# Kernel tuning notes

Hardware: AMD Instinct MI355X
Metric: run time of the kernel (lower is better)

The kernel has to match this reference:

```python
import jax, jax.numpy as jnp
import numpy as np


def _layernorm(x, g, b, eps=1e-5):
    m = jnp.mean(x, axis=-1, keepdims=True)
    v = jnp.var(x, axis=-1, keepdims=True)
    return (x - m) / jnp.sqrt(v + eps) * g + b


def _gat_layer(x, W, a1, a2, Wo, bo, diag_mask):
    # x: [B,N,D]; W: [H,D,D]; a1,a2: [H,D]; Wo: [H*D,D]; bo: [D]
    # Additive-attention split: a.[h_i;h_j] = a1.h_i + a2.h_j (same math as
    # the torch concat+linear, since the score layer is linear and bias-free).
    h = jnp.einsum('bni,hio->bhno', x, W)                       # [B,H,N,D]
    s1 = jnp.einsum('bhnd,hd->bhn', h, a1)                      # [B,H,N]
    s2 = jnp.einsum('bhnd,hd->bhn', h, a2)                      # [B,H,N]
    e = jax.nn.leaky_relu(s1[..., :, None] + s2[..., None, :], 0.2)  # [B,H,N,N]
    # fully-connected adjacency = ones - eye -> mask only the diagonal
    e = jnp.where(diag_mask, -jnp.inf, e)
    alpha = jax.nn.softmax(e, axis=-1)                          # [B,H,N,N]
    out = jnp.einsum('bhij,bhjd->bhid', alpha, h)               # [B,H,N,D]
    B, H, N, D = out.shape
    out = out.transpose(0, 2, 1, 3).reshape(B, N, H * D)        # concat heads
    return out @ Wo + bo                                        # [B,N,D]


def setup_inputs() -> dict:
    key = jax.random.key(0)
    ks = jax.random.split(key, 9)
    B, N, IN, D, H, L = 16, 1024, 7, 128, 4, 3
    s = 0.1
    return {
        'node_features': jax.random.normal(ks[0], (B, N, IN), jnp.float32),
        'Wp': jax.random.normal(ks[1], (IN, D), jnp.float32) * s,
        'bp': jax.random.normal(ks[2], (D,), jnp.float32) * s,
        'W':  jax.random.normal(ks[3], (L, H, D, D), jnp.float32) * s,
        'a1': jax.random.normal(ks[4], (L, H, D), jnp.float32) * s,
        'a2': jax.random.normal(ks[5], (L, H, D), jnp.float32) * s,
        'Wo': jax.random.normal(ks[6], (L, H * D, D), jnp.float32) * s,
        'bo': jax.random.normal(ks[7], (L, D), jnp.float32) * s,
        'gamma': jnp.ones((L, D), jnp.float32),
        'beta': jnp.zeros((L, D), jnp.float32),
    }


def reference(node_features, Wp, bp, W, a1, a2, Wo, bo, gamma, beta):
    B, N, _ = node_features.shape
    L = W.shape[0]
    diag_mask = jnp.eye(N, dtype=bool)  # adjacency==0 positions of (ones-eye)
    x = node_features @ Wp + bp         # input_proj
    for i in range(L):
        x_new = _gat_layer(x, W[i], a1[i], a2[i], Wo[i], bo[i], diag_mask)
        if i > 0:
            x = _layernorm(x + x_new, gamma[i], beta[i])  # residual + LN
        else:
            x = _layernorm(x_new, gamma[i], beta[i])
        if i < L - 1:
            x = jax.nn.relu(x)
    return x
```

## Files before the change

### kernel.cpp

```cpp
#include <hip/hip_runtime.h>
#include <hip/hip_bf16.h>

typedef __attribute__((ext_vector_type(8))) _Float16 f16x8;
typedef __attribute__((ext_vector_type(2))) _Float16 f16x2;
typedef __attribute__((ext_vector_type(8))) short short8;
typedef __attribute__((ext_vector_type(4))) short short4v;
typedef __attribute__((ext_vector_type(4))) float f32x4;

#define LDP 72
#define LDH 64

typedef const __attribute__((address_space(1))) unsigned int* gas_ptr;
typedef __attribute__((address_space(3))) unsigned int* las_ptr;
#define GLDS16(gp, lp) \
  __builtin_amdgcn_global_load_lds((gas_ptr)(gp), (las_ptr)(lp), 16, 0, 0)

#if __has_builtin(__builtin_amdgcn_fdot2)
#define FDOT2(a, b, c) __builtin_amdgcn_fdot2((a), (b), (c), false)
#else
__device__ __forceinline__ float FDOT2(f16x2 a, f16x2 b, float c) {
  return c + (float)a[0] * (float)b[0] + (float)a[1] * (float)b[1];
}
#endif

union h8u {
  f16x8 v;
  f16x2 h[4];
};

__device__ __forceinline__ short f2h(float f) {
  union { _Float16 h; short s; } u; u.h = (_Float16)f; return u.s;
}
__device__ __forceinline__ float h2f(short s) {
  union { short s; _Float16 h; } u; u.s = s; return (float)u.h;
}

__global__ __launch_bounds__(256) void k_tw(const float* __restrict__ W,
                                            const float* __restrict__ Wo,
                                            short* __restrict__ WT,
                                            short* __restrict__ WoT) {
  int idx = blockIdx.x * 256 + threadIdx.x;
  if (idx < 3 * 512 * 128) {
    int l = idx >> 16, rem = idx & 65535;
    int c = rem >> 7, k = rem & 127;
    int h = c >> 7, o = c & 127;
    WT[idx] = f2h(W[(((l * 4 + h) * 128 + k) << 7) + o]);
  } else {
    int j = idx - 3 * 512 * 128;
    int l = j >> 16, rem = j & 65535;
    int d = rem >> 9, c = rem & 511;
    WoT[j] = f2h(Wo[((l * 512 + c) << 7) + d]);
  }
}

__global__ __launch_bounds__(256) void k_inproj(const float* __restrict__ nf,
                                                const float* __restrict__ Wp,
                                                const float* __restrict__ bp,
                                                short* __restrict__ xh) {
  int idx = blockIdx.x * 256 + threadIdx.x;
  int bn = idx >> 7, d = idx & 127;
  float acc = bp[d];
  const float* nr = nf + bn * 7;
#pragma unroll
  for (int i = 0; i < 7; ++i) acc += nr[i] * Wp[(i << 7) + d];
  xh[idx] = f2h(acc);
}

__global__ __launch_bounds__(256) void k_gemm_h(const short* __restrict__ xh,
                                                const short* __restrict__ WT,
                                                short* __restrict__ hT,
                                                const float* __restrict__ a1,
                                                const float* __restrict__ a2,
                                                float* __restrict__ s1g,
                                                float* __restrict__ s2g) {
  __shared__ __align__(16) short As[128 * LDP];
  __shared__ __align__(16) short Bs[128 * LDP];
  __shared__ float sred[2][2][128];
  const int t = threadIdx.x;
  const int bn0 = blockIdx.x << 7;
  const int head = blockIdx.y;
  const int c0 = head << 7;
  const int w = t >> 6, lane = t & 63, lr = lane & 15, lq = lane >> 4;
  const int wr = w >> 1, wc = w & 1;
  f32x4 acc[4][4] = {};
  for (int k0 = 0; k0 < 128; k0 += 64) {
    const int row = t >> 1, half = (t & 1) << 5;
    {
      const short* sa = xh + ((bn0 + row) << 7) + k0 + half;
      short* da = As + row * LDP + half;
      *(short8*)(da) = *(const short8*)(sa);
      *(short8*)(da + 8) = *(const short8*)(sa + 8);
      *(short8*)(da + 16) = *(const short8*)(sa + 16);
      *(short8*)(da + 24) = *(const short8*)(sa + 24);
      const short* sb = WT + ((c0 + row) << 7) + k0 + half;
      short* db = Bs + row * LDP + half;
      *(short8*)(db) = *(const short8*)(sb);
      *(short8*)(db + 8) = *(const short8*)(sb + 8);
      *(short8*)(db + 16) = *(const short8*)(sb + 16);
      *(short8*)(db + 24) = *(const short8*)(sb + 24);
    }
    __syncthreads();
#pragma unroll
    for (int kk = 0; kk < 2; ++kk) {
      f16x8 a[4], b[4];
#pragma unroll
      for (int m = 0; m < 4; ++m)
        a[m] = *(const f16x8*)(As + (wr * 64 + m * 16 + lr) * LDP + (kk << 5) + (lq << 3));
#pragma unroll
      for (int n = 0; n < 4; ++n)
        b[n] = *(const f16x8*)(Bs + (wc * 64 + n * 16 + lr) * LDP + (kk << 5) + (lq << 3));
#pragma unroll
      for (int m = 0; m < 4; ++m)
#pragma unroll
        for (int n = 0; n < 4; ++n)
          acc[m][n] = __builtin_amdgcn_mfma_f32_16x16x32_f16(a[m], b[n], acc[m][n], 0, 0, 0);
    }
    __syncthreads();
  }
  const int b = bn0 >> 10;
  const int nb = bn0 & 1023;
  float a1v[4], a2v[4];
#pragma unroll
  for (int n = 0; n < 4; ++n) {
    int d = wc * 64 + n * 16 + lr;
    a1v[n] = a1[(head << 7) + d];
    a2v[n] = a2[(head << 7) + d];
  }
#pragma unroll
  for (int m = 0; m < 4; ++m)
#pragma unroll
    for (int r = 0; r < 4; ++r) {
      float v1 = 0.f, v2 = 0.f;
#pragma unroll
      for (int n = 0; n < 4; ++n) {
        v1 += acc[m][n][r] * a1v[n];
        v2 += acc[m][n][r] * a2v[n];
      }
#pragma unroll
      for (int off = 1; off < 16; off <<= 1) {
        v1 += __shfl_xor(v1, off);
        v2 += __shfl_xor(v2, off);
      }
      if (lr == 0) {
        int row = wr * 64 + m * 16 + (lq << 2) + r;
        sred[wc][0][row] = v1;
        sred[wc][1][row] = v2;
      }
    }
#pragma unroll
  for (int m = 0; m < 4; ++m) {
    int nrow = nb + wr * 64 + m * 16 + (lq << 2);
#pragma unroll
    for (int n = 0; n < 4; ++n) {
      int d = wc * 64 + n * 16 + lr;
      long base = ((long)((((b << 2) + head) << 7) + d) << 10) + nrow;
      short4v v;
      v[0] = f2h(acc[m][n][0]); v[1] = f2h(acc[m][n][1]);
      v[2] = f2h(acc[m][n][2]); v[3] = f2h(acc[m][n][3]);
      *(short4v*)(hT + base) = v;
    }
  }
  __syncthreads();
  {
    const int bh_ = (b << 2) + head;
    if (t < 128)
      s1g[(bh_ << 10) + nb + t] = sred[0][0][t] + sred[1][0][t];
    else
      s2g[(bh_ << 10) + nb + (t - 128)] = sred[0][1][t - 128] + sred[1][1][t - 128];
  }
}

__global__ __launch_bounds__(256) void k_ef(const float* __restrict__ s2g,
                                            float* __restrict__ s2m,
                                            short* __restrict__ Eh,
                                            short* __restrict__ Fh) {
  const int bh = blockIdx.x, t = threadIdx.x;
  __shared__ float red[4];
  f32x4 v = *(const f32x4*)&s2g[(bh << 10) + (t << 2)];
  float mx = fmaxf(fmaxf(v[0], v[1]), fmaxf(v[2], v[3]));
#pragma unroll
  for (int off = 1; off < 64; off <<= 1) mx = fmaxf(mx, __shfl_xor(mx, off));
  if ((t & 63) == 0) red[t >> 6] = mx;
  __syncthreads();
  const float smax = fmaxf(fmaxf(red[0], red[1]), fmaxf(red[2], red[3]));
  if (t == 0) s2m[bh] = smax;
  short4v e, f;
#pragma unroll
  for (int q = 0; q < 4; ++q) {
    e[q] = f2h(__expf(v[q] - smax));
    f[q] = f2h(__expf(0.2f * (v[q] - smax)));
  }
  *(short4v*)&Eh[(bh << 10) + (t << 2)] = e;
  *(short4v*)&Fh[(bh << 10) + (t << 2)] = f;
}

__global__ __launch_bounds__(256) void k_attn(const short* __restrict__ hT,
                                              const float* __restrict__ s1,
                                              const short* __restrict__ Eh,
                                              const short* __restrict__ Fh,
                                              const float* __restrict__ s2max,
                                              short* __restrict__ attn) {
  __shared__ __align__(16) short Hs[2][128 * LDH];
  __shared__ __align__(16) _Float16 Esh[1024];
  __shared__ __align__(16) _Float16 Fsh[1024];
  const int bh = blockIdx.x, it = blockIdx.y;
  const int i0 = it << 7;
  const int t = threadIdx.x;
  const int w = t >> 6, lane = t & 63, lr = lane & 15, lq = lane >> 4;

  const short* hTb = hT + ((long)bh << 17);
  const int grow = (w << 5) + (lane >> 3);
  const int gcol = ((lane & 7) ^ (lane >> 3)) << 3;
  const short* gsrc = hTb + ((long)grow << 10) + gcol;

#define STAGE(buf, J0)                                             \
  do {                                                             \
    short* ldsb = &Hs[buf][(w << 5) << 6];                         \
    _Pragma("unroll") for (int i_ = 0; i_ < 4; ++i_)               \
        GLDS16(gsrc + ((long)(i_ << 3) << 10) + (J0),              \
               ldsb + ((i_ << 3) << 6));                           \
  } while (0)

  STAGE(0, 0);
  *(short4v*)&Esh[t << 2] = *(const short4v*)&Eh[(bh << 10) + (t << 2)];
  *(short4v*)&Fsh[t << 2] = *(const short4v*)&Fh[(bh << 10) + (t << 2)];

  const float smax = s2max[bh];
  f16x8 Ai8[2], Bi8[2];
  const f16x2 one2 = {(_Float16)1.f, (_Float16)1.f};
  f16x8 dmask[2];
  float dsum[2] = {0.f, 0.f};
#pragma unroll
  for (int m = 0; m < 2; ++m) {
    const int rblk = (w << 5) + (m << 4) + lr;
    float s1v = s1[(bh << 10) + i0 + rblk];
    float x = s1v + smax;
    float mi = fmaxf(x, 0.2f * x);
    _Float16 A_ = (_Float16)__expf(x - mi);
    _Float16 B_ = (_Float16)__expf(0.2f * x - mi);
#pragma unroll
    for (int e = 0; e < 8; ++e) { Ai8[m][e] = A_; Bi8[m][e] = B_; }
    const int lqz = ((m << 1) + (lr >> 3)) & 3, ez = lr & 7;
#pragma unroll
    for (int e = 0; e < 8; ++e)
      dmask[m][e] = (lq == lqz && e == ez) ? (_Float16)0.f : (_Float16)1.f;
  }
  const int jtd = (it << 1) + (w >> 1);
  const int kkd = w & 1;
  f32x4 acc[2][8] = {};
  __syncthreads();

#define TILE(buf, jt, DIAG)                                                    \
  do {                                                                         \
    _Pragma("unroll") for (int kk = 0; kk < 2; ++kk) {                         \
      const int ebase = ((jt) << 6) + (kk << 5) + (lq << 3);                   \
      f16x8 ev8 = *(const f16x8*)&Esh[ebase];                                  \
      f16x8 fv8 = *(const f16x8*)&Fsh[ebase];                                  \
      f16x8 bf[8];                                                             \
      _Pragma("unroll") for (int n = 0; n < 8; ++n) {                          \
        const int r_ = (n << 4) + lr;                                          \
        const int slot_ = ((kk << 2) + lq) ^ (r_ & 7);                         \
        bf[n] = *(const f16x8*)(&Hs[buf][(r_ << 6) + (slot_ << 3)]);           \
      }                                                                        \
      f16x8 af[2];                                                             \
      _Pragma("unroll") for (int m = 0; m < 2; ++m) {                          \
        f16x8 pm = __builtin_elementwise_max(Ai8[m] * ev8, Bi8[m] * fv8);      \
        if ((DIAG) && kk == kkd) pm = pm * dmask[m];                           \
        af[m] = pm;                                                            \
        h8u u_; u_.v = pm;                                                     \
        _Pragma("unroll") for (int p = 0; p < 4; ++p)                          \
            dsum[m] = FDOT2(u_.h[p], one2, dsum[m]);                           \
      }                                                                        \
      _Pragma("unroll") for (int m = 0; m < 2; ++m)                            \
        _Pragma("unroll") for (int n = 0; n < 8; ++n)                          \
            acc[m][n] = __builtin_amdgcn_mfma_f32_16x16x32_f16(                \
                af[m], bf[n], acc[m][n], 0, 0, 0);                             \
    }                                                                          \
  } while (0)

#pragma unroll 1
  for (int jt2 = 0; jt2 < 8; ++jt2) {
    const int jA = jt2 << 1, jB = jA | 1;
    STAGE(1, jB << 6);
    __builtin_amdgcn_s_setprio(1);
    TILE(0, jA, jA == jtd);
    __builtin_amdgcn_s_setprio(0);
    __syncthreads();
    if (jt2 < 7) STAGE(0, (jA + 2) << 6);
    __builtin_amdgcn_s_setprio(1);
    TILE(1, jB, jB == jtd);
    __builtin_amdgcn_s_setprio(0);
    __syncthreads();
  }

  const int b = bh >> 2, head = bh & 3;
#pragma unroll
  for (int m = 0; m < 2; ++m) {
    float s = dsum[m];
    s += __shfl_xor(s, 16);
    s += __shfl_xor(s, 32);
    float rs = 1.f / s;
    f32x4 d4;
#pragma unroll
    for (int q = 0; q < 4; ++q)
      d4[q] = __shfl(rs, (lane & 48) | ((lq << 2) + q));
    int irow = i0 + (w << 5) + (m << 4) + (lq << 2);
#pragma unroll
    for (int n = 0; n < 8; ++n) {
      int d = (n << 4) + lr;
      long base = ((long)((b << 10) + irow) << 9) + (head << 7) + d;
      attn[base] = f2h(acc[m][n][0] * d4[0]);
      attn[base + 512] = f2h(acc[m][n][1] * d4[1]);
      attn[base + 1024] = f2h(acc[m][n][2] * d4[2]);
      attn[base + 1536] = f2h(acc[m][n][3] * d4[3]);
    }
  }
#undef STAGE
#undef TILE
}

template <int HAS_RES, int DO_RELU, int WRITE_OUT>
__global__ __launch_bounds__(256) void k_outproj(const short* __restrict__ attn,
                                                 const short* __restrict__ WoT,
                                                 const float* __restrict__ bo,
                                                 const float* __restrict__ gamma,
                                                 const float* __restrict__ beta,
                                                 float* __restrict__ xf,
                                                 short* __restrict__ xh,
                                                 float* __restrict__ outp) {
  __shared__ __align__(16) short As[64 * LDP];
  __shared__ __align__(16) short Bs[128 * LDP];
  const int t = threadIdx.x;
  const int bn0 = blockIdx.x << 6;
  const int w = t >> 6, lane = t & 63, lr = lane & 15, lq = lane >> 4;
  f32x4 acc[8] = {};
  const int rowA = t >> 2, chA = (t & 3) << 4;
  const int rowB = t >> 1, chB = (t & 1) << 5;
  for (int k0 = 0; k0 < 512; k0 += 64) {
    {
      const short* sa = attn + ((long)(bn0 + rowA) << 9) + k0 + chA;
      short* da = As + rowA * LDP + chA;
      *(short8*)(da) = *(const short8*)(sa);
      *(short8*)(da + 8) = *(const short8*)(sa + 8);
      const short* sb = WoT + (rowB << 9) + k0 + chB;
      short* db = Bs + rowB * LDP + chB;
      *(short8*)(db) = *(const short8*)(sb);
      *(short8*)(db + 8) = *(const short8*)(sb + 8);
      *(short8*)(db + 16) = *(const short8*)(sb + 16);
      *(short8*)(db + 24) = *(const short8*)(sb + 24);
    }
    __syncthreads();
#pragma unroll
    for (int kk = 0; kk < 2; ++kk) {
      f16x8 a = *(const f16x8*)(As + ((w << 4) + lr) * LDP + (kk << 5) + (lq << 3));
#pragma unroll
      for (int n = 0; n < 8; ++n) {
        f16x8 b = *(const f16x8*)(Bs + ((n << 4) + lr) * LDP + (kk << 5) + (lq << 3));
        acc[n] = __builtin_amdgcn_mfma_f32_16x16x32_f16(a, b, acc[n], 0, 0, 0);
      }
    }
    __syncthreads();
  }
  float v[8][4], gam[8], bet[8];
#pragma unroll
  for (int n = 0; n < 8; ++n) {
    int d = (n << 4) + lr;
    float bv = bo[d];
    gam[n] = gamma[d];
    bet[n] = beta[d];
#pragma unroll
    for (int r = 0; r < 4; ++r) {
      float x = acc[n][r] + bv;
      if (HAS_RES) x += xf[((bn0 + (w << 4) + (lq << 2) + r) << 7) + d];
      v[n][r] = x;
    }
  }
#pragma unroll
  for (int r = 0; r < 4; ++r) {
    float s = 0.f, q = 0.f;
#pragma unroll
    for (int n = 0; n < 8; ++n) { s += v[n][r]; q += v[n][r] * v[n][r]; }
#pragma unroll
    for (int mk = 1; mk < 16; mk <<= 1) { s += __shfl_xor(s, mk); q += __shfl_xor(q, mk); }
    float mean = s * 0.0078125f;
    float var = q * 0.0078125f - mean * mean;
    float rstd = rsqrtf(var + 1e-5f);
    int row = bn0 + (w << 4) + (lq << 2) + r;
#pragma unroll
    for (int n = 0; n < 8; ++n) {
      int d = (n << 4) + lr;
      float o = (v[n][r] - mean) * rstd * gam[n] + bet[n];
      if (DO_RELU) o = fmaxf(o, 0.f);
      if (WRITE_OUT) {
        outp[(row << 7) + d] = o;
      } else {
        xh[(row << 7) + d] = f2h(o);
        xf[(row << 7) + d] = o;
      }
    }
  }
}

extern "C" void kernel_launch(void* const* d_in, const int* in_sizes, int n_in,
                              void* d_out, int out_size, void* d_ws, size_t ws_size,
                              hipStream_t stream) {
  const float* nf = (const float*)d_in[0];
  const float* Wp = (const float*)d_in[1];
  const float* bp = (const float*)d_in[2];
  const float* W = (const float*)d_in[3];
  const float* a1 = (const float*)d_in[4];
  const float* a2 = (const float*)d_in[5];
  const float* Wo = (const float*)d_in[6];
  const float* bo = (const float*)d_in[7];
  const float* gamma = (const float*)d_in[8];
  const float* beta = (const float*)d_in[9];
  float* outp = (float*)d_out;

  char* ws = (char*)d_ws;
  short* xh = (short*)(ws);
  float* xf = (float*)(ws + (4ll << 20));
  short* hT = (short*)(ws + (12ll << 20));
  short* attn = (short*)(ws + (28ll << 20));
  float* s1 = (float*)(ws + (44ll << 20));
  float* s2g = (float*)(ws + (44ll << 20) + (256ll << 10));
  short* Eh = (short*)(ws + (44ll << 20) + (512ll << 10));
  short* Fh = (short*)(ws + (44ll << 20) + (640ll << 10));
  float* s2m = (float*)(ws + (44ll << 20) + (768ll << 10));
  short* WT = (short*)(ws + (45ll << 20));
  short* WoT = (short*)(ws + (45ll << 20) + 393216);

  k_tw<<<1536, 256, 0, stream>>>(W, Wo, WT, WoT);
  k_inproj<<<8192, 256, 0, stream>>>(nf, Wp, bp, xh);
  for (int l = 0; l < 3; ++l) {
    k_gemm_h<<<dim3(128, 4), 256, 0, stream>>>(xh, WT + l * 65536, hT,
                                               a1 + l * 512, a2 + l * 512, s1, s2g);
    k_ef<<<64, 256, 0, stream>>>(s2g, s2m, Eh, Fh);
    k_attn<<<dim3(64, 8), 256, 0, stream>>>(hT, s1, Eh, Fh, s2m, attn);
    if (l == 0)
      k_outproj<0, 1, 0><<<256, 256, 0, stream>>>(attn, WoT + l * 65536, bo + l * 128,
                                                  gamma + l * 128, beta + l * 128, xf, xh, outp);
    else if (l == 1)
      k_outproj<1, 1, 0><<<256, 256, 0, stream>>>(attn, WoT + l * 65536, bo + l * 128,
                                                  gamma + l * 128, beta + l * 128, xf, xh, outp);
    else
      k_outproj<1, 0, 1><<<256, 256, 0, stream>>>(attn, WoT + l * 65536, bo + l * 128,
                                                  gamma + l * 128, beta + l * 128, xf, xh, outp);
  }
}
```

Baseline: 170.8 us.

## Triple-buffer attention H tiles and split outproj rows across more blocks

The attention kernel moves from double to triple buffering of the H tiles in LDS. It prefetches two tiles ahead and replaces __syncthreads with explicit vmcnt waits and raw barriers, so global-to-LDS loads overlap more MFMA work. The output projection kernel halves the rows per block, from 64 to 32, and splits the 128 output columns across wave pairs. The LayerNorm statistics are then combined through shared memory, and twice as many blocks are launched. The changes trade extra LDS use and an added cross-wave reduction barrier for deeper latency hiding and better occupancy across CUs.

```diff
diff --git a/kernel.cpp b/kernel.cpp
--- a/kernel.cpp
+++ b/kernel.cpp
@@ -200,7 +200,7 @@
                                               const short* __restrict__ Fh,
                                               const float* __restrict__ s2max,
                                               short* __restrict__ attn) {
-  __shared__ __align__(16) short Hs[2][128 * LDH];
+  __shared__ __align__(16) short Hs[3][128 * LDH];
   __shared__ __align__(16) _Float16 Esh[1024];
   __shared__ __align__(16) _Float16 Fsh[1024];
   const int bh = blockIdx.x, it = blockIdx.y;
@@ -222,6 +222,7 @@
   } while (0)
 
   STAGE(0, 0);
+  STAGE(1, 64);
   *(short4v*)&Esh[t << 2] = *(const short4v*)&Eh[(bh << 10) + (t << 2)];
   *(short4v*)&Fsh[t << 2] = *(const short4v*)&Fh[(bh << 10) + (t << 2)];
 
@@ -278,19 +279,23 @@
     }                                                                          \
   } while (0)
 
+  int cur = 0;
 #pragma unroll 1
-  for (int jt2 = 0; jt2 < 8; ++jt2) {
-    const int jA = jt2 << 1, jB = jA | 1;
-    STAGE(1, jB << 6);
+  for (int jt = 0; jt < 16; ++jt) {
+    if (jt < 14) {
+      STAGE((cur == 0 ? 2 : cur - 1), (jt + 2) << 6);
+      asm volatile("s_waitcnt vmcnt(8)" ::: "memory");
+    } else if (jt == 14) {
+      asm volatile("s_waitcnt vmcnt(4)" ::: "memory");
+    } else {
+      asm volatile("s_waitcnt vmcnt(0)" ::: "memory");
+    }
+    __builtin_amdgcn_s_barrier();
     __builtin_amdgcn_s_setprio(1);
-    TILE(0, jA, jA == jtd);
+    TILE(cur, jt, jt == jtd);
     __builtin_amdgcn_s_setprio(0);
-    __syncthreads();
-    if (jt2 < 7) STAGE(0, (jA + 2) << 6);
-    __builtin_amdgcn_s_setprio(1);
-    TILE(1, jB, jB == jtd);
-    __builtin_amdgcn_s_setprio(0);
-    __syncthreads();
+    __builtin_amdgcn_s_barrier();
+    cur = (cur == 2) ? 0 : cur + 1;
   }
 
   const int b = bh >> 2, head = bh & 3;
@@ -328,20 +333,20 @@
                                                  float* __restrict__ xf,
                                                  short* __restrict__ xh,
                                                  float* __restrict__ outp) {
-  __shared__ __align__(16) short As[64 * LDP];
+  __shared__ __align__(16) short As[32 * LDP];
   __shared__ __align__(16) short Bs[128 * LDP];
+  __shared__ float sredS[2][32], sredQ[2][32];
   const int t = threadIdx.x;
-  const int bn0 = blockIdx.x << 6;
+  const int bn0 = blockIdx.x << 5;
   const int w = t >> 6, lane = t & 63, lr = lane & 15, lq = lane >> 4;
-  f32x4 acc[8] = {};
-  const int rowA = t >> 2, chA = (t & 3) << 4;
+  const int wm = w & 1, wn = w >> 1;
+  f32x4 acc[4] = {};
+  const int rowA = t >> 3, chA = (t & 7) << 3;
   const int rowB = t >> 1, chB = (t & 1) << 5;
   for (int k0 = 0; k0 < 512; k0 += 64) {
     {
       const short* sa = attn + ((long)(bn0 + rowA) << 9) + k0 + chA;
-      short* da = As + rowA * LDP + chA;
-      *(short8*)(da) = *(const short8*)(sa);
-      *(short8*)(da + 8) = *(const short8*)(sa + 8);
+      *(short8*)(As + rowA * LDP + chA) = *(const short8*)(sa);
       const short* sb = WoT + (rowB << 9) + k0 + chB;
       short* db = Bs + rowB * LDP + chB;
       *(short8*)(db) = *(const short8*)(sb);
@@ -352,44 +357,56 @@
     __syncthreads();
 #pragma unroll
     for (int kk = 0; kk < 2; ++kk) {
-      f16x8 a = *(const f16x8*)(As + ((w << 4) + lr) * LDP + (kk << 5) + (lq << 3));
-#pragma unroll
-      for (int n = 0; n < 8; ++n) {
-        f16x8 b = *(const f16x8*)(Bs + ((n << 4) + lr) * LDP + (kk << 5) + (lq << 3));
-        acc[n] = __builtin_amdgcn_mfma_f32_16x16x32_f16(a, b, acc[n], 0, 0, 0);
+      f16x8 a = *(const f16x8*)(As + ((wm << 4) + lr) * LDP + (kk << 5) + (lq << 3));
+#pragma unroll
+      for (int nn = 0; nn < 4; ++nn) {
+        f16x8 b = *(const f16x8*)(Bs + ((wn << 6) + (nn << 4) + lr) * LDP + (kk << 5) + (lq << 3));
+        acc[nn] = __builtin_amdgcn_mfma_f32_16x16x32_f16(a, b, acc[nn], 0, 0, 0);
       }
     }
     __syncthreads();
   }
-  float v[8][4], gam[8], bet[8];
-#pragma unroll
-  for (int n = 0; n < 8; ++n) {
-    int d = (n << 4) + lr;
+  float v[4][4], gam[4], bet[4];
+#pragma unroll
+  for (int nn = 0; nn < 4; ++nn) {
+    int d = (wn << 6) + (nn << 4) + lr;
     float bv = bo[d];
-    gam[n] = gamma[d];
-    bet[n] = beta[d];
+    gam[nn] = gamma[d];
+    bet[nn] = beta[d];
 #pragma unroll
     for (int r = 0; r < 4; ++r) {
-      float x = acc[n][r] + bv;
-      if (HAS_RES) x += xf[((bn0 + (w << 4) + (lq << 2) + r) << 7) + d];
-      v[n][r] = x;
+      float x = acc[nn][r] + bv;
+      if (HAS_RES) x += xf[((bn0 + (wm << 4) + (lq << 2) + r) << 7) + d];
+      v[nn][r] = x;
     }
   }
 #pragma unroll
   for (int r = 0; r < 4; ++r) {
     float s = 0.f, q = 0.f;
 #pragma unroll
-    for (int n = 0; n < 8; ++n) { s += v[n][r]; q += v[n][r] * v[n][r]; }
+    for (int nn = 0; nn < 4; ++nn) { s += v[nn][r]; q += v[nn][r] * v[nn][r]; }
 #pragma unroll
     for (int mk = 1; mk < 16; mk <<= 1) { s += __shfl_xor(s, mk); q += __shfl_xor(q, mk); }
-    float mean = s * 0.0078125f;
-    float var = q * 0.0078125f - mean * mean;
+    if (lr == 0) {
+      int row = (wm << 4) + (lq << 2) + r;
+      sredS[wn][row] = s;
+      sredQ[wn][row] = q;
+    }
+  }
+  __syncthreads();
+#pragma unroll
+  for (int r = 0; r < 4; ++r) {
+    int rloc = (wm << 4) + (lq << 2) + r;
+    float S = sredS[0][rloc] + sredS[1][rloc];
+    float Q = sredQ[0][rloc] + sredQ[1][rloc];
+    float mean = S * 0.0078125f;
+    float var = Q * 0.0078125f - mean * mean;
     float rstd = rsqrtf(var + 1e-5f);
-    int row = bn0 + (w << 4) + (lq << 2) + r;
-#pragma unroll
-    for (int n = 0; n < 8; ++n) {
-      int d = (n << 4) + lr;
-      float o = (v[n][r] - mean) * rstd * gam[n] + bet[n];
+    int row = bn0 + rloc;
+#pragma unroll
+    for (int nn = 0; nn < 4; ++nn) {
+      int d = (wn << 6) + (nn << 4) + lr;
+      float o = (v[nn][r] - mean) * rstd * gam[nn] + bet[nn];
       if (DO_RELU) o = fmaxf(o, 0.f);
       if (WRITE_OUT) {
         outp[(row << 7) + d] = o;
@@ -437,13 +454,13 @@
     k_ef<<<64, 256, 0, stream>>>(s2g, s2m, Eh, Fh);
     k_attn<<<dim3(64, 8), 256, 0, stream>>>(hT, s1, Eh, Fh, s2m, attn);
     if (l == 0)
-      k_outproj<0, 1, 0><<<256, 256, 0, stream>>>(attn, WoT + l * 65536, bo + l * 128,
+      k_outproj<0, 1, 0><<<512, 256, 0, stream>>>(attn, WoT + l * 65536, bo + l * 128,
                                                   gamma + l * 128, beta + l * 128, xf, xh, outp);
     else if (l == 1)
-      k_outproj<1, 1, 0><<<256, 256, 0, stream>>>(attn, WoT + l * 65536, bo + l * 128,
+      k_outproj<1, 1, 0><<<512, 256, 0, stream>>>(attn, WoT + l * 65536, bo + l * 128,
                                                   gamma + l * 128, beta + l * 128, xf, xh, outp);
     else
-      k_outproj<1, 0, 1><<<256, 256, 0, stream>>>(attn, WoT + l * 65536, bo + l * 128,
+      k_outproj<1, 0, 1><<<512, 256, 0, stream>>>(attn, WoT + l * 65536, bo + l * 128,
                                                   gamma + l * 128, beta + l * 128, xf, xh, outp);
   }
 }
```

Measured after the change: 163.8 us. -4.1%, faster.
